# Optimization experiments

Measured on AMD Instinct MI355X. Metric: run time of the kernel, lower is better.

## Reference

```python
import jax, jax.numpy as jnp
import numpy as np

S = 14          # grid size
B = 2           # boxes per cell
NCLS = 20       # number of classes
L_COORD = 5.0
L_NOOBJ = 0.5


def setup_inputs() -> dict:
    key = jax.random.key(0)
    k1, k2, k3, k4 = jax.random.split(key, 4)
    N = 4096
    pred_tensor = jax.random.uniform(k1, (N, S, S, B * 5 + NCLS), dtype=jnp.float32)
    target_boxes = jax.random.uniform(k2, (N, S, S, 4), dtype=jnp.float32)
    target_cls = jax.random.uniform(k3, (N, S, S, NCLS), dtype=jnp.float32)
    has_object_map = jax.random.randint(k4, (N, S, S), 0, 2) == 1
    return {
        "pred_tensor": pred_tensor,
        "target_boxes": target_boxes,
        "target_cls": target_cls,
        "has_object_map": has_object_map,
    }


def _yolo_loss(pred_tensor, target_boxes, target_cls, has_object_map):
    N = pred_tensor.shape[0]
    inv_n = 1.0 / N
    m = has_object_map.astype(pred_tensor.dtype)            # (N,S,S) 1 where object

    pred_boxes = pred_tensor[..., : B * 5].reshape(*pred_tensor.shape[:3], B, 5)  # (N,S,S,B,5)
    pred_cls = pred_tensor[..., B * 5:]                     # (N,S,S,20)

    # class loss over object cells (masked sum == boolean-index + sum)
    cls_loss = jnp.sum(m[..., None] * (pred_cls - target_cls) ** 2) * inv_n

    # no-object confidence loss: all B confidences at non-object cells vs 0
    conf = pred_boxes[..., 4]                               # (N,S,S,B)
    no_obj_loss = jnp.sum((1.0 - m)[..., None] * conf ** 2) * inv_n

    # per-cell IoU of each of the B predicted boxes against the target box.
    # xywh2xyxy: center x,y are divided by S; w,h used directly (as in source).
    xy = pred_boxes[..., :2] / S                            # (N,S,S,B,2)
    wh = pred_boxes[..., 2:4]                               # (N,S,S,B,2)
    p1 = xy - wh / 2
    p2 = xy + wh / 2
    t = target_boxes[..., None, :]                          # (N,S,S,1,4) treated as xyxy
    lt = jnp.maximum(p1, t[..., :2])
    rb = jnp.minimum(p2, t[..., 2:])
    iwh = jnp.clip(rb - lt, 0.0)
    inter = iwh[..., 0] * iwh[..., 1]                       # (N,S,S,B)
    area_p = wh[..., 0] * wh[..., 1]                        # (x2-x1)*(y2-y1) = w*h
    area_t = (t[..., 2] - t[..., 0]) * (t[..., 3] - t[..., 1])
    iou = inter / (area_p + area_t - inter)                 # (N,S,S,B)

    # best-of-B selection per cell (torch.max picks first max index -> argmax)
    best_idx = jnp.argmax(iou, axis=-1)                     # (N,S,S)
    best_boxes = jnp.take_along_axis(
        pred_boxes, best_idx[..., None, None], axis=3
    )[..., 0, :]                                            # (N,S,S,5)

    # containing-object confidence loss: best conf vs 1.0 at object cells
    containing_obj_loss = jnp.sum(m * (best_boxes[..., 4] - 1.0) ** 2) * inv_n

    center_loss = jnp.sum(m[..., None] * (best_boxes[..., :2] - target_boxes[..., :2]) ** 2)
    dim_loss = jnp.sum(
        m[..., None]
        * (jnp.sqrt(best_boxes[..., 2:4]) - jnp.sqrt(target_boxes[..., 2:4])) ** 2
    )
    reg_loss = (center_loss + dim_loss) * inv_n

    total_loss = cls_loss + L_NOOBJ * no_obj_loss + L_COORD * reg_loss + containing_obj_loss
    # [total, reg, containing_obj, no_obj, cls]
    return jnp.stack([total_loss, reg_loss, containing_obj_loss, no_obj_loss, cls_loss])


def reference(pred_tensor, target_boxes, target_cls, has_object_map):
    return _yolo_loss(pred_tensor, target_boxes, target_cls, has_object_map)
```

## Files before the change

### kernel.cpp

```cpp
#include <hip/hip_runtime.h>


#define NCELLS (4096 * 14 * 14)
#define NBLOCKS (NCELLS / 256)


__global__ void yolo_zero_kernel(float* __restrict__ ws) {
    if (threadIdx.x < 16) ws[threadIdx.x] = 0.0f;
}

__global__ void yolo_detect_kernel(const unsigned char* __restrict__ mb,
                                   int* __restrict__ flag) {
    int t = threadIdx.x;
    unsigned int found = 0;
#pragma unroll
    for (int k = 0; k < 16; ++k) {
        int slot = t * 16 + k;
        found |= mb[4 * slot + 1] | mb[4 * slot + 2] | mb[4 * slot + 3];
    }
    if (found) atomicOr(flag, 1);
}

__global__ __launch_bounds__(256) void yolo_main_kernel(
    const float* __restrict__ pred,
    const float* __restrict__ tbox,
    const float* __restrict__ tcls,
    const void* __restrict__ mask,
    const int* __restrict__ flag,
    float* __restrict__ ws) {
    const int c = blockIdx.x * 256 + threadIdx.x;

    float pv[30];
    {
        const float2* p2 = (const float2*)(pred + (long long)30 * c);
#pragma unroll
        for (int k = 0; k < 15; ++k) {
            float2 t = p2[k];
            pv[2 * k] = t.x;
            pv[2 * k + 1] = t.y;
        }
    }
    const float4 tb = *(const float4*)(tbox + (long long)4 * c);
    float tc[20];
    {
        const float4* c4 = (const float4*)(tcls + (long long)20 * c);
#pragma unroll
        for (int k = 0; k < 5; ++k) {
            float4 t = c4[k];
            tc[4 * k] = t.x;
            tc[4 * k + 1] = t.y;
            tc[4 * k + 2] = t.z;
            tc[4 * k + 3] = t.w;
        }
    }
    const int mode = *flag;
    float m;
    if (mode) {
        m = ((const unsigned char*)mask)[c] ? 1.0f : 0.0f;
    } else {
        m = ((const int*)mask)[c] ? 1.0f : 0.0f;
    }

    float s = 0.0f;
#pragma unroll
    for (int i = 0; i < 20; ++i) {
        float d = pv[10 + i] - tc[i];
        s += d * d;
    }
    float cls_s = m * s;

    float conf0 = pv[4], conf1 = pv[9];
    float noobj_s = (1.0f - m) * (conf0 * conf0 + conf1 * conf1);

    float iou[2];
    float at = (tb.z - tb.x) * (tb.w - tb.y);
#pragma unroll
    for (int b = 0; b < 2; ++b) {
        int base = 5 * b;
        float x = pv[base] / 14.0f;
        float y = pv[base + 1] / 14.0f;
        float w = pv[base + 2];
        float h = pv[base + 3];
        float p1x = x - w * 0.5f, p1y = y - h * 0.5f;
        float p2x = x + w * 0.5f, p2y = y + h * 0.5f;
        float ltx = fmaxf(p1x, tb.x), lty = fmaxf(p1y, tb.y);
        float rbx = fminf(p2x, tb.z), rby = fminf(p2y, tb.w);
        float iw = fmaxf(rbx - ltx, 0.0f), ih = fmaxf(rby - lty, 0.0f);
        float inter = iw * ih;
        float ap = w * h;
        iou[b] = inter / (ap + at - inter);
    }
    int best = (iou[1] > iou[0]) ? 5 : 0;
    float bx = pv[best], by = pv[best + 1], bw = pv[best + 2], bh = pv[best + 3],
          bc = pv[best + 4];

    float contain_s = m * (bc - 1.0f) * (bc - 1.0f);

    float dx = bx - tb.x, dy = by - tb.y;
    float dw = sqrtf(bw) - sqrtf(tb.z);
    float dh = sqrtf(bh) - sqrtf(tb.w);
    float reg_s = m * (dx * dx + dy * dy + dw * dw + dh * dh);

#pragma unroll
    for (int off = 32; off > 0; off >>= 1) {
        cls_s += __shfl_down(cls_s, off, 64);
        noobj_s += __shfl_down(noobj_s, off, 64);
        contain_s += __shfl_down(contain_s, off, 64);
        reg_s += __shfl_down(reg_s, off, 64);
    }
    __shared__ float red[4][4];
    int lane = threadIdx.x & 63;
    int wid = threadIdx.x >> 6;
    if (lane == 0) {
        red[wid][0] = cls_s;
        red[wid][1] = noobj_s;
        red[wid][2] = contain_s;
        red[wid][3] = reg_s;
    }
    __syncthreads();
    if (threadIdx.x < 4) {
        float v = red[0][threadIdx.x] + red[1][threadIdx.x] +
                  red[2][threadIdx.x] + red[3][threadIdx.x];
        atomicAdd(&ws[threadIdx.x], v);
    }
}

__global__ void yolo_final_kernel(const float* __restrict__ ws,
                                  float* __restrict__ out) {
    if (threadIdx.x == 0) {
        const float inv_n = 1.0f / 4096.0f;
        float cls = ws[0] * inv_n;
        float noobj = ws[1] * inv_n;
        float contain = ws[2] * inv_n;
        float reg = ws[3] * inv_n;
        float total = cls + 0.5f * noobj + 5.0f * reg + contain;
        out[0] = total;
        out[1] = reg;
        out[2] = contain;
        out[3] = noobj;
        out[4] = cls;
    }
}

extern "C" void kernel_launch(void* const* d_in, const int* in_sizes, int n_in,
                              void* d_out, int out_size, void* d_ws,
                              size_t ws_size, hipStream_t stream) {
    const float* pred = (const float*)d_in[0];
    const float* tbox = (const float*)d_in[1];
    const float* tcls = (const float*)d_in[2];
    const void* mask = d_in[3];
    float* ws = (float*)d_ws;
    float* out = (float*)d_out;

    yolo_zero_kernel<<<1, 64, 0, stream>>>(ws);
    yolo_detect_kernel<<<1, 256, 0, stream>>>((const unsigned char*)mask,
                                              (int*)(ws + 8));
    yolo_main_kernel<<<NBLOCKS, 256, 0, stream>>>(pred, tbox, tcls, mask,
                                                  (const int*)(ws + 8), ws);
    yolo_final_kernel<<<1, 64, 0, stream>>>(ws, out);
}
```

Baseline: 208.5 us.

## Stage pred/cls through LDS with coalesced loads and fuse kernel launches

The main kernel now loads each block's contiguous pred and target-class rows into shared memory with coalesced float4 loads, then reads each cell's values from LDS. Before, each thread did strided per-thread vector loads. The zero and detect kernels are merged into one init kernel, and the final kernel is removed by having the last block, found through an atomic counter, finalize the output. Together these cut launch overhead and improve global memory coalescing, at the cost of about 50KB of LDS per block, which lowers occupancy.

```diff
diff --git a/kernel.cpp b/kernel.cpp
--- a/kernel.cpp
+++ b/kernel.cpp
@@ -2,15 +2,13 @@
 
 
 #define NCELLS (4096 * 14 * 14)
-#define NBLOCKS (NCELLS / 256)
+#define TPB 256
+#define NBLOCKS (NCELLS / TPB)
 
 
-__global__ void yolo_zero_kernel(float* __restrict__ ws) {
+__global__ void yolo_init_kernel(float* ws, const unsigned char* mb) {
     if (threadIdx.x < 16) ws[threadIdx.x] = 0.0f;
-}
-
-__global__ void yolo_detect_kernel(const unsigned char* __restrict__ mb,
-                                   int* __restrict__ flag) {
+    __syncthreads();
     int t = threadIdx.x;
     unsigned int found = 0;
 #pragma unroll
@@ -18,7 +16,7 @@
         int slot = t * 16 + k;
         found |= mb[4 * slot + 1] | mb[4 * slot + 2] | mb[4 * slot + 3];
     }
-    if (found) atomicOr(flag, 1);
+    if (found) atomicOr((int*)(ws + 8), 1);
 }
 
 __global__ __launch_bounds__(256) void yolo_main_kernel(
@@ -26,13 +24,40 @@
     const float* __restrict__ tbox,
     const float* __restrict__ tcls,
     const void* __restrict__ mask,
-    const int* __restrict__ flag,
-    float* __restrict__ ws) {
-    const int c = blockIdx.x * 256 + threadIdx.x;
+    float* ws,
+    float* __restrict__ out) {
+    __shared__ float sp[TPB * 30];
+    __shared__ float sc[TPB * 20];
+    const int tid = threadIdx.x;
+    const int blk = blockIdx.x;
+    const int c = blk * TPB + tid;
+
+    {
+        const float4* gp = (const float4*)(pred + (size_t)blk * (TPB * 30));
+        float4* lp = (float4*)sp;
+#pragma unroll
+        for (int j = 0; j < 7; ++j) lp[tid + 256 * j] = gp[tid + 256 * j];
+        if (tid < 128) lp[tid + 1792] = gp[tid + 1792];
+        const float4* gc = (const float4*)(tcls + (size_t)blk * (TPB * 20));
+        float4* lc = (float4*)sc;
+#pragma unroll
+        for (int j = 0; j < 5; ++j) lc[tid + 256 * j] = gc[tid + 256 * j];
+    }
+
+    const float4 tb = ((const float4*)tbox)[c];
+    const int mode = ((const int*)(ws + 8))[0];
+    float m;
+    if (mode) {
+        m = ((const unsigned char*)mask)[c] ? 1.0f : 0.0f;
+    } else {
+        m = ((const int*)mask)[c] ? 1.0f : 0.0f;
+    }
+
+    __syncthreads();
 
     float pv[30];
     {
-        const float2* p2 = (const float2*)(pred + (long long)30 * c);
+        const float2* p2 = (const float2*)(sp + tid * 30);
 #pragma unroll
         for (int k = 0; k < 15; ++k) {
             float2 t = p2[k];
@@ -40,10 +65,9 @@
             pv[2 * k + 1] = t.y;
         }
     }
-    const float4 tb = *(const float4*)(tbox + (long long)4 * c);
     float tc[20];
     {
-        const float4* c4 = (const float4*)(tcls + (long long)20 * c);
+        const float4* c4 = (const float4*)(sc + tid * 20);
 #pragma unroll
         for (int k = 0; k < 5; ++k) {
             float4 t = c4[k];
@@ -52,13 +76,6 @@
             tc[4 * k + 2] = t.z;
             tc[4 * k + 3] = t.w;
         }
-    }
-    const int mode = *flag;
-    float m;
-    if (mode) {
-        m = ((const unsigned char*)mask)[c] ? 1.0f : 0.0f;
-    } else {
-        m = ((const int*)mask)[c] ? 1.0f : 0.0f;
     }
 
     float s = 0.0f;
@@ -77,8 +94,8 @@
 #pragma unroll
     for (int b = 0; b < 2; ++b) {
         int base = 5 * b;
-        float x = pv[base] / 14.0f;
-        float y = pv[base + 1] / 14.0f;
+        float x = pv[base] * (1.0f / 14.0f);
+        float y = pv[base + 1] * (1.0f / 14.0f);
         float w = pv[base + 2];
         float h = pv[base + 3];
         float p1x = x - w * 0.5f, p1y = y - h * 0.5f;
@@ -91,8 +108,8 @@
         iou[b] = inter / (ap + at - inter);
     }
     int best = (iou[1] > iou[0]) ? 5 : 0;
-    float bx = pv[best], by = pv[best + 1], bw = pv[best + 2], bh = pv[best + 3],
-          bc = pv[best + 4];
+    float bx = pv[best], by = pv[best + 1], bw = pv[best + 2],
+          bh = pv[best + 3], bc = pv[best + 4];
 
     float contain_s = m * (bc - 1.0f) * (bc - 1.0f);
 
@@ -109,8 +126,8 @@
         reg_s += __shfl_down(reg_s, off, 64);
     }
     __shared__ float red[4][4];
-    int lane = threadIdx.x & 63;
-    int wid = threadIdx.x >> 6;
+    int lane = tid & 63;
+    int wid = tid >> 6;
     if (lane == 0) {
         red[wid][0] = cls_s;
         red[wid][1] = noobj_s;
@@ -118,27 +135,28 @@
         red[wid][3] = reg_s;
     }
     __syncthreads();
-    if (threadIdx.x < 4) {
-        float v = red[0][threadIdx.x] + red[1][threadIdx.x] +
-                  red[2][threadIdx.x] + red[3][threadIdx.x];
-        atomicAdd(&ws[threadIdx.x], v);
+    if (tid < 4) {
+        float v = red[0][tid] + red[1][tid] + red[2][tid] + red[3][tid];
+        atomicAdd(&ws[tid], v);
     }
-}
+    __syncthreads();
 
-__global__ void yolo_final_kernel(const float* __restrict__ ws,
-                                  float* __restrict__ out) {
-    if (threadIdx.x == 0) {
-        const float inv_n = 1.0f / 4096.0f;
-        float cls = ws[0] * inv_n;
-        float noobj = ws[1] * inv_n;
-        float contain = ws[2] * inv_n;
-        float reg = ws[3] * inv_n;
-        float total = cls + 0.5f * noobj + 5.0f * reg + contain;
-        out[0] = total;
-        out[1] = reg;
-        out[2] = contain;
-        out[3] = noobj;
-        out[4] = cls;
+    if (tid == 0) {
+        __threadfence();
+        unsigned int prev = atomicAdd((unsigned int*)(ws + 4), 1u);
+        if (prev == (unsigned int)(NBLOCKS - 1)) {
+            __threadfence();
+            const float inv_n = 1.0f / 4096.0f;
+            float cls = atomicAdd(&ws[0], 0.0f) * inv_n;
+            float noobj = atomicAdd(&ws[1], 0.0f) * inv_n;
+            float contain = atomicAdd(&ws[2], 0.0f) * inv_n;
+            float reg = atomicAdd(&ws[3], 0.0f) * inv_n;
+            out[0] = cls + 0.5f * noobj + 5.0f * reg + contain;
+            out[1] = reg;
+            out[2] = contain;
+            out[3] = noobj;
+            out[4] = cls;
+        }
     }
 }
 
@@ -152,10 +170,7 @@
     float* ws = (float*)d_ws;
     float* out = (float*)d_out;
 
-    yolo_zero_kernel<<<1, 64, 0, stream>>>(ws);
-    yolo_detect_kernel<<<1, 256, 0, stream>>>((const unsigned char*)mask,
-                                              (int*)(ws + 8));
-    yolo_main_kernel<<<NBLOCKS, 256, 0, stream>>>(pred, tbox, tcls, mask,
-                                                  (const int*)(ws + 8), ws);
-    yolo_final_kernel<<<1, 64, 0, stream>>>(ws, out);
+    yolo_init_kernel<<<1, 256, 0, stream>>>(ws, (const unsigned char*)mask);
+    yolo_main_kernel<<<NBLOCKS, TPB, 0, stream>>>(pred, tbox, tcls, mask, ws,
+                                                  out);
 }
```

Result: slower. 303.6 us (+45.6%).
